# Kernel optimization log

Measured on AMD Instinct MI355X. Metric: run time of the kernel, lower is better.

## Reference

```python
import jax, jax.numpy as jnp
import numpy as np

D_MODEL = 2048
NUM_HEADS = 32
NUM_GROUPS = 8
HEAD_DIM = D_MODEL // NUM_HEADS  # 64
HEADS_PER_GROUP = NUM_HEADS // NUM_GROUPS  # 4


def setup_inputs() -> dict:
    key = jax.random.key(0)
    ks = jax.random.split(key, 5)
    B, S = 1, 2048
    x = jax.random.normal(ks[0], (B, S, D_MODEL), dtype=jnp.float32)
    scale = 1.0 / np.sqrt(D_MODEL)
    w_q = jax.random.normal(ks[1], (D_MODEL, D_MODEL), dtype=jnp.float32) * scale
    w_k = jax.random.normal(ks[2], (D_MODEL, NUM_GROUPS * HEAD_DIM), dtype=jnp.float32) * scale
    w_v = jax.random.normal(ks[3], (D_MODEL, NUM_GROUPS * HEAD_DIM), dtype=jnp.float32) * scale
    w_o = jax.random.normal(ks[4], (D_MODEL, D_MODEL), dtype=jnp.float32) * scale
    return {"x": x, "w_q": w_q, "w_k": w_k, "w_v": w_v, "w_o": w_o}


def reference(x, w_q, w_k, w_v, w_o):
    B, S, _ = x.shape
    # projections (nn.Linear, no bias)
    q = (x @ w_q).reshape(B, S, NUM_HEADS, HEAD_DIM)          # [B,S,H,d]
    k = (x @ w_k).reshape(B, S, NUM_GROUPS, HEAD_DIM)         # [B,S,G,d]
    v = (x @ w_v).reshape(B, S, NUM_GROUPS, HEAD_DIM)
    # group queries: [B,S,G,hpg,d] so each KV group serves heads_per_group query heads
    qg = q.reshape(B, S, NUM_GROUPS, HEADS_PER_GROUP, HEAD_DIM)
    scale = 1.0 / jnp.sqrt(jnp.asarray(HEAD_DIM, dtype=x.dtype))
    # scores: [B,G,hpg,S_q,S_k] without duplicating K/V
    scores = jnp.einsum("bsghd,btgd->bghst", qg, k) * scale
    attn = jax.nn.softmax(scores, axis=-1)
    out = jnp.einsum("bghst,btgd->bsghd", attn, v)            # [B,S,G,hpg,d]
    out = out.reshape(B, S, D_MODEL)
    return out @ w_o
```

## Files before the change

### kernel.cpp

```cpp
#include <hip/hip_runtime.h>

typedef unsigned short ushort_t;
typedef __attribute__((ext_vector_type(8))) short short8;
typedef __attribute__((ext_vector_type(4))) float floatx4;

__device__ __forceinline__ unsigned short f2bf(float f) {
  unsigned int u = __float_as_uint(f);
  u += 0x7fffu + ((u >> 16) & 1u);
  return (unsigned short)(u >> 16);
}

__device__ __forceinline__ unsigned int cvt_pk_bf16(float a, float b) {
  unsigned int r;
  asm("v_cvt_pk_bf16_f32 %0, %1, %2" : "=v"(r) : "v"(a), "v"(b));
  return r;
}

__device__ __forceinline__ void gl_lds16(const void* g, void* l) {
  __builtin_amdgcn_global_load_lds((const __attribute__((address_space(1))) void*)g,
                                   (__attribute__((address_space(3))) void*)l,
                                   16, 0, 0);
}


__global__ void conv_x_kernel(const float* __restrict__ src, ushort_t* __restrict__ dst, int n4) {
  int i = blockIdx.x * blockDim.x + threadIdx.x;
  if (i >= n4) return;
  float4 v = ((const float4*)src)[i];
  union { ushort_t u[4]; unsigned long long ll; } o;
  o.u[0] = f2bf(v.x); o.u[1] = f2bf(v.y); o.u[2] = f2bf(v.z); o.u[3] = f2bf(v.w);
  ((unsigned long long*)dst)[i] = o.ll;
}

__global__ void transpose_conv(const float* __restrict__ src, ushort_t* __restrict__ dst,
                               int R, int C) {
  __shared__ float tile[32][33];
  int c0 = blockIdx.x * 32, r0 = blockIdx.y * 32;
  int tx = threadIdx.x, ty = threadIdx.y;
#pragma unroll
  for (int i = ty; i < 32; i += 8)
    tile[i][tx] = src[(long)(r0 + i) * C + c0 + tx];
  __syncthreads();
#pragma unroll
  for (int i = ty; i < 32; i += 8)
    dst[(long)(c0 + i) * R + r0 + tx] = f2bf(tile[tx][i]);
}

template <int EPI>
__global__ __launch_bounds__(256, 2) void gemm_bt(
    const ushort_t* __restrict__ A, const ushort_t* __restrict__ B,
    float* __restrict__ C,
    ushort_t* __restrict__ qb, ushort_t* __restrict__ kb, ushort_t* __restrict__ vb,
    int M, int N, int K) {
  __shared__ ushort_t As[128 * 32];
  __shared__ ushort_t Bs[128 * 32];
  const int t = threadIdx.x;
  const int w = t >> 6, lane = t & 63;
  const int m = lane & 15, quad = lane >> 4;
  const int m0 = blockIdx.y * 128, n0 = blockIdx.x * 128;
  const int wr = w >> 1, wc = w & 1;

  floatx4 acc[4][4] = {};

  for (int kk = 0; kk < K; kk += 32) {
    __syncthreads();
#pragma unroll
    for (int i = 0; i < 2; ++i) {
      int c = i * 256 + t;
      int c0 = i * 256 + w * 64;
      gl_lds16(A + (long)(m0 + (c >> 2)) * K + kk + (c & 3) * 8, As + c0 * 8);
      gl_lds16(B + (long)(n0 + (c >> 2)) * K + kk + (c & 3) * 8, Bs + c0 * 8);
    }
    __syncthreads();
    short8 af[4], bf[4];
#pragma unroll
    for (int i = 0; i < 4; ++i)
      af[i] = *(const short8*)(As + (wr * 64 + i * 16 + m) * 32 + quad * 8);
#pragma unroll
    for (int j = 0; j < 4; ++j)
      bf[j] = *(const short8*)(Bs + (wc * 64 + j * 16 + m) * 32 + quad * 8);
#pragma unroll
    for (int i = 0; i < 4; ++i)
#pragma unroll
      for (int j = 0; j < 4; ++j)
        acc[i][j] = __builtin_amdgcn_mfma_f32_16x16x32_bf16(af[i], bf[j], acc[i][j], 0, 0, 0);
  }

#pragma unroll
  for (int i = 0; i < 4; ++i)
#pragma unroll
    for (int j = 0; j < 4; ++j)
#pragma unroll
      for (int r = 0; r < 4; ++r) {
        float v = acc[i][j][r];
        int row = m0 + wr * 64 + i * 16 + quad * 4 + r;
        int col = n0 + wc * 64 + j * 16 + m;
        if (EPI == 1) {
          C[(long)row * N + col] = v;
        } else {
          if (col < 2048) {
            qb[((((col >> 6) * 2048) + row) << 6) | (col & 63)] = f2bf(v * 0.18033688f);
          } else if (col < 2560) {
            int g = (col - 2048) >> 6;
            kb[(((g * 2048) + row) << 6) | (col & 63)] = f2bf(v);
          } else {
            int g = (col - 2560) >> 6;
            vb[(long)((g << 6) | (col & 63)) * 2048 + row] = f2bf(v);
          }
        }
      }
}

__global__ __launch_bounds__(256, 2) void flash_kernel(
    const ushort_t* __restrict__ Q, const ushort_t* __restrict__ Kb,
    const ushort_t* __restrict__ Vb, ushort_t* __restrict__ O, int S) {
  __shared__ __attribute__((aligned(16))) ushort_t Ks[2 * 128 * 32];
  __shared__ __attribute__((aligned(16))) ushort_t Vs[4 * 64 * 32];
  __shared__ __attribute__((aligned(16))) ushort_t Ps[4 * 32 * 64];
  const int t = threadIdx.x;
  const int w = t >> 6, lane = t & 63;
  const int m = lane & 15, quad = lane >> 4;
  const int h = blockIdx.y, g = h >> 2;
  const int q0 = blockIdx.x * 128;
  const ushort_t* qp = Q + (long)h * S * 64;
  const ushort_t* kp = Kb + (long)g * S * 64;
  const ushort_t* vp = Vb + (long)g * 64 * S;

  short8 qf[2][2];
#pragma unroll
  for (int rt = 0; rt < 2; ++rt)
#pragma unroll
    for (int kq = 0; kq < 2; ++kq)
      qf[rt][kq] = *(const short8*)(qp + (long)(q0 + w * 32 + rt * 16 + m) * 64 + kq * 32 + quad * 8);

  float mcur[2] = {-1e30f, -1e30f};
  float lcur[2] = {0.f, 0.f};
  floatx4 oacc[2][4] = {};
  char* PwB = (char*)Ps + w * 4096;
  const int swz = (m & 7) << 4;
  const int kvswz = (quad ^ ((m >> 1) & 3)) * 8;

  for (int t0 = 0; t0 < S; t0 += 128) {
    __syncthreads();
#pragma unroll
    for (int i = 0; i < 4; ++i) {
      int c = i * 256 + t;
      int c0 = i * 256 + w * 64;
      int sl = ((c & 3) ^ ((c >> 3) & 3)) * 8;
      gl_lds16(kp + (long)(t0 + ((c >> 2) & 127)) * 64 + (c >> 9) * 32 + sl, Ks + c0 * 8);
      gl_lds16(vp + (long)((c >> 2) & 63) * S + t0 + (c >> 8) * 32 + sl, Vs + c0 * 8);
    }
    __syncthreads();

    floatx4 sacc[2][8] = {};
    __builtin_amdgcn_s_setprio(1);
#pragma unroll
    for (int ct = 0; ct < 8; ++ct) {
      short8 kf0 = *(const short8*)(Ks + (ct * 16 + m) * 32 + kvswz);
      short8 kf1 = *(const short8*)(Ks + 4096 + (ct * 16 + m) * 32 + kvswz);
#pragma unroll
      for (int rt = 0; rt < 2; ++rt) {
        sacc[rt][ct] = __builtin_amdgcn_mfma_f32_16x16x32_bf16(kf0, qf[rt][0], sacc[rt][ct], 0, 0, 0);
        sacc[rt][ct] = __builtin_amdgcn_mfma_f32_16x16x32_bf16(kf1, qf[rt][1], sacc[rt][ct], 0, 0, 0);
      }
    }
    __builtin_amdgcn_s_setprio(0);

    float mnew[2], al[2];
#pragma unroll
    for (int rt = 0; rt < 2; ++rt) {
      float mt[8];
#pragma unroll
      for (int ct = 0; ct < 8; ++ct)
        mt[ct] = fmaxf(fmaxf(sacc[rt][ct][0], sacc[rt][ct][1]),
                       fmaxf(sacc[rt][ct][2], sacc[rt][ct][3]));
      float mx = fmaxf(fmaxf(fmaxf(mt[0], mt[1]), fmaxf(mt[2], mt[3])),
                       fmaxf(fmaxf(mt[4], mt[5]), fmaxf(mt[6], mt[7])));
      mx = fmaxf(mx, __shfl_xor(mx, 16));
      mx = fmaxf(mx, __shfl_xor(mx, 32));
      mnew[rt] = fmaxf(mcur[rt], mx);
      al[rt] = exp2f(mcur[rt] - mnew[rt]);
      mcur[rt] = mnew[rt];
    }

#pragma unroll
    for (int rt = 0; rt < 2; ++rt)
#pragma unroll
      for (int r = 0; r < 4; ++r) {
        float alr = __shfl(al[rt], quad * 4 + r);
#pragma unroll
        for (int ct = 0; ct < 4; ++ct) oacc[rt][ct][r] *= alr;
      }

    float ls[2] = {0.f, 0.f};
#pragma unroll
    for (int hh = 0; hh < 2; ++hh) {
#pragma unroll
      for (int rt = 0; rt < 2; ++rt)
#pragma unroll
        for (int cl = 0; cl < 4; ++cl) {
          int ct = hh * 4 + cl;
          float p0 = exp2f(sacc[rt][ct][0] - mnew[rt]);
          float p1 = exp2f(sacc[rt][ct][1] - mnew[rt]);
          float p2 = exp2f(sacc[rt][ct][2] - mnew[rt]);
          float p3 = exp2f(sacc[rt][ct][3] - mnew[rt]);
          ls[rt] += (p0 + p1) + (p2 + p3);
          uint2 pk;
          pk.x = cvt_pk_bf16(p0, p1);
          pk.y = cvt_pk_bf16(p2, p3);
          *(uint2*)(PwB + ((rt * 2048 + m * 128 + cl * 32 + quad * 8) ^ swz)) = pk;
        }
      __builtin_amdgcn_s_setprio(1);
#pragma unroll
      for (int ktl = 0; ktl < 2; ++ktl) {
        int kt = hh * 2 + ktl;
        short8 pf[2];
#pragma unroll
        for (int rt = 0; rt < 2; ++rt)
          pf[rt] = *(const short8*)(PwB + ((rt * 2048 + m * 128 + ktl * 64 + quad * 16) ^ swz));
#pragma unroll
        for (int ct = 0; ct < 4; ++ct) {
          short8 vf = *(const short8*)(Vs + kt * 2048 + (ct * 16 + m) * 32 + kvswz);
#pragma unroll
          for (int rt = 0; rt < 2; ++rt)
            oacc[rt][ct] = __builtin_amdgcn_mfma_f32_16x16x32_bf16(pf[rt], vf, oacc[rt][ct], 0, 0, 0);
        }
      }
      __builtin_amdgcn_s_setprio(0);
    }

#pragma unroll
    for (int rt = 0; rt < 2; ++rt) {
      float s_ = ls[rt];
      s_ += __shfl_xor(s_, 16);
      s_ += __shfl_xor(s_, 32);
      lcur[rt] = lcur[rt] * al[rt] + s_;
    }
  }

#pragma unroll
  for (int rt = 0; rt < 2; ++rt) {
    float linv = 1.f / lcur[rt];
#pragma unroll
    for (int r = 0; r < 4; ++r) {
      float lr = __shfl(linv, quad * 4 + r);
      int srow = q0 + w * 32 + rt * 16 + quad * 4 + r;
#pragma unroll
      for (int ct = 0; ct < 4; ++ct)
        O[(long)srow * 2048 + h * 64 + ct * 16 + m] = f2bf(oacc[rt][ct][r] * lr);
    }
  }
}


extern "C" void kernel_launch(void* const* d_in, const int* in_sizes, int n_in,
                              void* d_out, int out_size, void* d_ws, size_t ws_size,
                              hipStream_t stream) {
  (void)in_sizes; (void)n_in; (void)out_size; (void)ws_size;
  const float* x  = (const float*)d_in[0];
  const float* wq = (const float*)d_in[1];
  const float* wk = (const float*)d_in[2];
  const float* wv = (const float*)d_in[3];
  const float* wo = (const float*)d_in[4];
  float* out = (float*)d_out;
  char* ws = (char*)d_ws;
  const size_t MB = 1u << 20;

  ushort_t* xb    = (ushort_t*)(ws);
  ushort_t* wqkvT = (ushort_t*)(ws + 8 * MB);
  ushort_t* woT   = (ushort_t*)(ws + 20 * MB);
  ushort_t* qbuf  = (ushort_t*)(ws + 28 * MB);
  ushort_t* kbuf  = (ushort_t*)(ws + 36 * MB);
  ushort_t* vbuf  = (ushort_t*)(ws + 38 * MB);
  ushort_t* attn  = xb;

  conv_x_kernel<<<4096, 256, 0, stream>>>(x, xb, 2048 * 2048 / 4);
  dim3 tb(32, 8);
  transpose_conv<<<dim3(64, 64), tb, 0, stream>>>(wq, wqkvT, 2048, 2048);
  transpose_conv<<<dim3(16, 64), tb, 0, stream>>>(wk, wqkvT + 2048 * 2048, 2048, 512);
  transpose_conv<<<dim3(16, 64), tb, 0, stream>>>(wv, wqkvT + 2560 * 2048, 2048, 512);
  transpose_conv<<<dim3(64, 64), tb, 0, stream>>>(wo, woT, 2048, 2048);

  gemm_bt<0><<<dim3(24, 16), 256, 0, stream>>>(xb, wqkvT, nullptr, qbuf, kbuf, vbuf,
                                               2048, 3072, 2048);
  flash_kernel<<<dim3(16, 32), 256, 0, stream>>>(qbuf, kbuf, vbuf, attn, 2048);
  gemm_bt<1><<<dim3(16, 16), 256, 0, stream>>>(attn, woT, out, nullptr, nullptr, nullptr,
                                               2048, 2048, 2048);
}
```

Before: 281.5 us.

## Double-buffer GEMM and flash LDS tiles, swizzle blocks, lazy rescale, MFMA row sums

Both the GEMM and the flash-attention kernel now double-buffer their LDS tiles, so the next K/V or A/B tile is fetched while MFMAs run on the current one, with one barrier per iteration. Workgroup IDs are remapped in groups of eight to change cache locality. Flash attention skips the softmax rescale when the running max grows by at most 8 (log2 units) across the wave, and computes row sums with an MFMA against a ones vector instead of shuffles. LDS use roughly doubles, which may lower occupancy. The lazy-max threshold lets unnormalised exponentials reach up to 2^8 in bf16.

```diff
diff --git a/kernel.cpp b/kernel.cpp
--- a/kernel.cpp
+++ b/kernel.cpp
@@ -52,38 +52,48 @@
     float* __restrict__ C,
     ushort_t* __restrict__ qb, ushort_t* __restrict__ kb, ushort_t* __restrict__ vb,
     int M, int N, int K) {
-  __shared__ ushort_t As[128 * 32];
-  __shared__ ushort_t Bs[128 * 32];
+  __shared__ __attribute__((aligned(16))) ushort_t As[2][128 * 32];
+  __shared__ __attribute__((aligned(16))) ushort_t Bs[2][128 * 32];
   const int t = threadIdx.x;
   const int w = t >> 6, lane = t & 63;
   const int m = lane & 15, quad = lane >> 4;
-  const int m0 = blockIdx.y * 128, n0 = blockIdx.x * 128;
+  const int nwg = gridDim.x * gridDim.y;
+  const int bid = blockIdx.y * gridDim.x + blockIdx.x;
+  const int sw = (bid & 7) * (nwg >> 3) + (bid >> 3);
+  const int m0 = (sw / gridDim.x) * 128, n0 = (sw % gridDim.x) * 128;
   const int wr = w >> 1, wc = w & 1;
 
   floatx4 acc[4][4] = {};
 
-  for (int kk = 0; kk < K; kk += 32) {
-    __syncthreads();
+  auto stage = [&](int kk, int buf) {
 #pragma unroll
     for (int i = 0; i < 2; ++i) {
       int c = i * 256 + t;
       int c0 = i * 256 + w * 64;
-      gl_lds16(A + (long)(m0 + (c >> 2)) * K + kk + (c & 3) * 8, As + c0 * 8);
-      gl_lds16(B + (long)(n0 + (c >> 2)) * K + kk + (c & 3) * 8, Bs + c0 * 8);
-    }
-    __syncthreads();
+      gl_lds16(A + (long)(m0 + (c >> 2)) * K + kk + (c & 3) * 8, As[buf] + c0 * 8);
+      gl_lds16(B + (long)(n0 + (c >> 2)) * K + kk + (c & 3) * 8, Bs[buf] + c0 * 8);
+    }
+  };
+
+  stage(0, 0);
+  __syncthreads();
+  int cur = 0;
+  for (int kk = 0; kk < K; kk += 32) {
+    if (kk + 32 < K) stage(kk + 32, cur ^ 1);
     short8 af[4], bf[4];
 #pragma unroll
     for (int i = 0; i < 4; ++i)
-      af[i] = *(const short8*)(As + (wr * 64 + i * 16 + m) * 32 + quad * 8);
+      af[i] = *(const short8*)(As[cur] + (wr * 64 + i * 16 + m) * 32 + quad * 8);
 #pragma unroll
     for (int j = 0; j < 4; ++j)
-      bf[j] = *(const short8*)(Bs + (wc * 64 + j * 16 + m) * 32 + quad * 8);
+      bf[j] = *(const short8*)(Bs[cur] + (wc * 64 + j * 16 + m) * 32 + quad * 8);
 #pragma unroll
     for (int i = 0; i < 4; ++i)
 #pragma unroll
       for (int j = 0; j < 4; ++j)
         acc[i][j] = __builtin_amdgcn_mfma_f32_16x16x32_bf16(af[i], bf[j], acc[i][j], 0, 0, 0);
+    __syncthreads();
+    cur ^= 1;
   }
 
 #pragma unroll
@@ -114,18 +124,34 @@
 __global__ __launch_bounds__(256, 2) void flash_kernel(
     const ushort_t* __restrict__ Q, const ushort_t* __restrict__ Kb,
     const ushort_t* __restrict__ Vb, ushort_t* __restrict__ O, int S) {
-  __shared__ __attribute__((aligned(16))) ushort_t Ks[2 * 128 * 32];
-  __shared__ __attribute__((aligned(16))) ushort_t Vs[4 * 64 * 32];
+  __shared__ __attribute__((aligned(16))) ushort_t Ks[2][128 * 64];
+  __shared__ __attribute__((aligned(16))) ushort_t Vs[2][128 * 64];
   __shared__ __attribute__((aligned(16))) ushort_t Ps[4 * 32 * 64];
   const int t = threadIdx.x;
   const int w = t >> 6, lane = t & 63;
   const int m = lane & 15, quad = lane >> 4;
-  const int h = blockIdx.y, g = h >> 2;
-  const int q0 = blockIdx.x * 128;
+  const int nwg = gridDim.x * gridDim.y;
+  const int bid = blockIdx.y * gridDim.x + blockIdx.x;
+  const int sw = (bid & 7) * (nwg >> 3) + (bid >> 3);
+  const int h = sw / gridDim.x, g = h >> 2;
+  const int q0 = (sw % gridDim.x) * 128;
   const ushort_t* qp = Q + (long)h * S * 64;
   const ushort_t* kp = Kb + (long)g * S * 64;
   const ushort_t* vp = Vb + (long)g * 64 * S;
 
+  auto stage = [&](int t0, int buf) {
+#pragma unroll
+    for (int i = 0; i < 4; ++i) {
+      int c = i * 256 + t;
+      int c0 = i * 256 + w * 64;
+      int sl = ((c & 3) ^ ((c >> 3) & 3)) * 8;
+      gl_lds16(kp + (long)(t0 + ((c >> 2) & 127)) * 64 + (c >> 9) * 32 + sl, Ks[buf] + c0 * 8);
+      gl_lds16(vp + (long)((c >> 2) & 63) * S + t0 + (c >> 8) * 32 + sl, Vs[buf] + c0 * 8);
+    }
+  };
+
+  stage(0, 0);
+
   short8 qf[2][2];
 #pragma unroll
   for (int rt = 0; rt < 2; ++rt)
@@ -133,31 +159,28 @@
     for (int kq = 0; kq < 2; ++kq)
       qf[rt][kq] = *(const short8*)(qp + (long)(q0 + w * 32 + rt * 16 + m) * 64 + kq * 32 + quad * 8);
 
+  short8 ones;
+#pragma unroll
+  for (int z = 0; z < 8; ++z) ones[z] = (short)0x3F80;
+
   float mcur[2] = {-1e30f, -1e30f};
-  float lcur[2] = {0.f, 0.f};
+  floatx4 lacc[2] = {};
   floatx4 oacc[2][4] = {};
   char* PwB = (char*)Ps + w * 4096;
   const int swz = (m & 7) << 4;
   const int kvswz = (quad ^ ((m >> 1) & 3)) * 8;
 
+  __syncthreads();
+  int cur = 0;
   for (int t0 = 0; t0 < S; t0 += 128) {
-    __syncthreads();
-#pragma unroll
-    for (int i = 0; i < 4; ++i) {
-      int c = i * 256 + t;
-      int c0 = i * 256 + w * 64;
-      int sl = ((c & 3) ^ ((c >> 3) & 3)) * 8;
-      gl_lds16(kp + (long)(t0 + ((c >> 2) & 127)) * 64 + (c >> 9) * 32 + sl, Ks + c0 * 8);
-      gl_lds16(vp + (long)((c >> 2) & 63) * S + t0 + (c >> 8) * 32 + sl, Vs + c0 * 8);
-    }
-    __syncthreads();
+    if (t0 + 128 < S) stage(t0 + 128, cur ^ 1);
 
     floatx4 sacc[2][8] = {};
     __builtin_amdgcn_s_setprio(1);
 #pragma unroll
     for (int ct = 0; ct < 8; ++ct) {
-      short8 kf0 = *(const short8*)(Ks + (ct * 16 + m) * 32 + kvswz);
-      short8 kf1 = *(const short8*)(Ks + 4096 + (ct * 16 + m) * 32 + kvswz);
+      short8 kf0 = *(const short8*)(Ks[cur] + (ct * 16 + m) * 32 + kvswz);
+      short8 kf1 = *(const short8*)(Ks[cur] + 4096 + (ct * 16 + m) * 32 + kvswz);
 #pragma unroll
       for (int rt = 0; rt < 2; ++rt) {
         sacc[rt][ct] = __builtin_amdgcn_mfma_f32_16x16x32_bf16(kf0, qf[rt][0], sacc[rt][ct], 0, 0, 0);
@@ -166,7 +189,7 @@
     }
     __builtin_amdgcn_s_setprio(0);
 
-    float mnew[2], al[2];
+    float mnew[2];
 #pragma unroll
     for (int rt = 0; rt < 2; ++rt) {
       float mt[8];
@@ -178,21 +201,31 @@
                        fmaxf(fmaxf(mt[4], mt[5]), fmaxf(mt[6], mt[7])));
       mx = fmaxf(mx, __shfl_xor(mx, 16));
       mx = fmaxf(mx, __shfl_xor(mx, 32));
-      mnew[rt] = fmaxf(mcur[rt], mx);
-      al[rt] = exp2f(mcur[rt] - mnew[rt]);
-      mcur[rt] = mnew[rt];
-    }
-
-#pragma unroll
-    for (int rt = 0; rt < 2; ++rt)
-#pragma unroll
-      for (int r = 0; r < 4; ++r) {
-        float alr = __shfl(al[rt], quad * 4 + r);
-#pragma unroll
-        for (int ct = 0; ct < 4; ++ct) oacc[rt][ct][r] *= alr;
+      mnew[rt] = mx;
+    }
+
+    if (__all((mnew[0] - mcur[0] <= 8.f) && (mnew[1] - mcur[1] <= 8.f))) {
+      mnew[0] = mcur[0];
+      mnew[1] = mcur[1];
+    } else {
+      float al[2];
+#pragma unroll
+      for (int rt = 0; rt < 2; ++rt) {
+        mnew[rt] = fmaxf(mcur[rt], mnew[rt]);
+        al[rt] = exp2f(mcur[rt] - mnew[rt]);
+        mcur[rt] = mnew[rt];
       }
-
-    float ls[2] = {0.f, 0.f};
+#pragma unroll
+      for (int rt = 0; rt < 2; ++rt)
+#pragma unroll
+        for (int r = 0; r < 4; ++r) {
+          float alr = __shfl(al[rt], quad * 4 + r);
+          lacc[rt][r] *= alr;
+#pragma unroll
+          for (int ct = 0; ct < 4; ++ct) oacc[rt][ct][r] *= alr;
+        }
+    }
+
 #pragma unroll
     for (int hh = 0; hh < 2; ++hh) {
 #pragma unroll
@@ -204,7 +237,6 @@
           float p1 = exp2f(sacc[rt][ct][1] - mnew[rt]);
           float p2 = exp2f(sacc[rt][ct][2] - mnew[rt]);
           float p3 = exp2f(sacc[rt][ct][3] - mnew[rt]);
-          ls[rt] += (p0 + p1) + (p2 + p3);
           uint2 pk;
           pk.x = cvt_pk_bf16(p0, p1);
           pk.y = cvt_pk_bf16(p2, p3);
@@ -216,11 +248,13 @@
         int kt = hh * 2 + ktl;
         short8 pf[2];
 #pragma unroll
-        for (int rt = 0; rt < 2; ++rt)
+        for (int rt = 0; rt < 2; ++rt) {
           pf[rt] = *(const short8*)(PwB + ((rt * 2048 + m * 128 + ktl * 64 + quad * 16) ^ swz));
+          lacc[rt] = __builtin_amdgcn_mfma_f32_16x16x32_bf16(pf[rt], ones, lacc[rt], 0, 0, 0);
+        }
 #pragma unroll
         for (int ct = 0; ct < 4; ++ct) {
-          short8 vf = *(const short8*)(Vs + kt * 2048 + (ct * 16 + m) * 32 + kvswz);
+          short8 vf = *(const short8*)(Vs[cur] + kt * 2048 + (ct * 16 + m) * 32 + kvswz);
 #pragma unroll
           for (int rt = 0; rt < 2; ++rt)
             oacc[rt][ct] = __builtin_amdgcn_mfma_f32_16x16x32_bf16(pf[rt], vf, oacc[rt][ct], 0, 0, 0);
@@ -229,27 +263,20 @@
       __builtin_amdgcn_s_setprio(0);
     }
 
-#pragma unroll
-    for (int rt = 0; rt < 2; ++rt) {
-      float s_ = ls[rt];
-      s_ += __shfl_xor(s_, 16);
-      s_ += __shfl_xor(s_, 32);
-      lcur[rt] = lcur[rt] * al[rt] + s_;
-    }
+    __syncthreads();
+    cur ^= 1;
   }
 
 #pragma unroll
-  for (int rt = 0; rt < 2; ++rt) {
-    float linv = 1.f / lcur[rt];
+  for (int rt = 0; rt < 2; ++rt)
 #pragma unroll
     for (int r = 0; r < 4; ++r) {
-      float lr = __shfl(linv, quad * 4 + r);
+      float inv = 1.f / lacc[rt][r];
       int srow = q0 + w * 32 + rt * 16 + quad * 4 + r;
 #pragma unroll
       for (int ct = 0; ct < 4; ++ct)
-        O[(long)srow * 2048 + h * 64 + ct * 16 + m] = f2bf(oacc[rt][ct][r] * lr);
-    }
-  }
+        O[(long)srow * 2048 + h * 64 + ct * 16 + m] = f2bf(oacc[rt][ct][r] * inv);
+    }
 }
 
 
```

Measured after the change: 272.6 us. 1.03x faster.
